# Kernel optimization log

Hardware: AMD Instinct MI355X
Metric: run time of the kernel (lower is better)

Reference implementation:

```python
import jax, jax.numpy as jnp
import numpy as np

N = 100000       # num nodes
E = 3200000      # num edges (avg degree 32)
F_IN = 128       # num_node_features
HID = 16         # hidden dim hard-coded in Net
C = 10           # num_classes


def setup_inputs() -> dict:
    key = jax.random.key(0)
    k1, k2, k3, k4 = jax.random.split(key, 4)
    x = jax.random.normal(k1, (N, F_IN), dtype=jnp.float32)
    edge_index = jax.random.randint(k2, (2, E), 0, N, dtype=jnp.int32)
    W1 = jax.random.normal(k3, (F_IN, HID), dtype=jnp.float32) * 0.05
    b1 = jnp.zeros((HID,), dtype=jnp.float32)
    W2 = jax.random.normal(k4, (HID, C), dtype=jnp.float32) * 0.05
    b2 = jnp.zeros((C,), dtype=jnp.float32)
    return {"x": x, "edge_index": edge_index, "W1": W1, "b1": b1, "W2": W2, "b2": b2}


def reference(x, edge_index, W1, b1, W2, b2):
    # GCNConv: out = D^{-1/2} (A + I) D^{-1/2} X W + b   (add self-loops)
    loops = jnp.arange(N, dtype=edge_index.dtype)
    row = jnp.concatenate([edge_index[0], loops])  # source nodes
    col = jnp.concatenate([edge_index[1], loops])  # target nodes

    # symmetric normalization (degrees include self-loops, so deg >= 1)
    deg = jax.ops.segment_sum(jnp.ones_like(col, dtype=jnp.float32), col, num_segments=N)
    dis = jax.lax.rsqrt(deg)
    norm = dis[row] * dis[col]  # [E+N]

    def gcn_conv(h, W, b):
        h = h @ W                               # [N, d_out] small GEMM first
        msg = h[row] * norm[:, None]            # gather + scale, [E+N, d_out]
        out = jax.ops.segment_sum(msg, col, num_segments=N)  # scatter-add
        return out + b

    h = jax.nn.relu(gcn_conv(x, W1, b1))
    # F.dropout(training=False) is identity in eval mode
    logits = gcn_conv(h, W2, b2)
    return jax.nn.log_softmax(logits, axis=1)
```

## Files before the change

kernel.cpp:

```cpp
#include <hip/hip_runtime.h>
#include <math.h>

#define N_NODES 100000
#define N_EDGES 3200000
#define F_IN 128
#define HID 16
#define C_OUT 10
#define WIN 256
#define NDIG 391
#define PNB2 500
#define EPB 6400
#define SCN (NDIG * PNB2)
#define SB1 764
#define MAXE2 20

typedef unsigned short u16;
typedef unsigned int u32;

__device__ __forceinline__ float bf2f(u16 u) {
    return __uint_as_float(((u32)u) << 16);
}
__device__ __forceinline__ u16 f2bf(float f) {
    u32 x = __float_as_uint(f);
    u32 r = (x + 0x7fffu + ((x >> 16) & 1u)) >> 16;
    return (u16)r;
}
__device__ __forceinline__ void acc8(float* a, uint4 w) {
    a[0] += bf2f((u16)(w.x & 0xffff)); a[1] += bf2f((u16)(w.x >> 16));
    a[2] += bf2f((u16)(w.y & 0xffff)); a[3] += bf2f((u16)(w.y >> 16));
    a[4] += bf2f((u16)(w.z & 0xffff)); a[5] += bf2f((u16)(w.z >> 16));
    a[6] += bf2f((u16)(w.w & 0xffff)); a[7] += bf2f((u16)(w.w >> 16));
}

__global__ void k_pcnt(const int* __restrict__ col, int* __restrict__ blkhistA) {
    __shared__ int h[NDIG];
    for (int i = threadIdx.x; i < NDIG; i += 256) h[i] = 0;
    __syncthreads();
    const uint4* c4 = (const uint4*)(col + blockIdx.x * EPB);
    for (int i = threadIdx.x; i < EPB / 4; i += 256) {
        uint4 c = c4[i];
        atomicAdd(&h[c.x >> 8], 1);
        atomicAdd(&h[c.y >> 8], 1);
        atomicAdd(&h[c.z >> 8], 1);
        atomicAdd(&h[c.w >> 8], 1);
    }
    __syncthreads();
    for (int d = threadIdx.x; d < NDIG; d += 256)
        blkhistA[d * PNB2 + blockIdx.x] = h[d];
}

__global__ void k_s1(const int* __restrict__ blkhistA, int* __restrict__ psum) {
    __shared__ int sm[256];
    int i = blockIdx.x * 256 + threadIdx.x;
    sm[threadIdx.x] = (i < SCN) ? blkhistA[i] : 0;
    __syncthreads();
    for (int off = 128; off > 0; off >>= 1) {
        if (threadIdx.x < off) sm[threadIdx.x] += sm[threadIdx.x + off];
        __syncthreads();
    }
    if (threadIdx.x == 0) psum[blockIdx.x] = sm[0];
}

__global__ void k_s3(const int* __restrict__ blkhistA, const int* __restrict__ psum,
                     int* __restrict__ blkhistB) {
    __shared__ int ps[1024];
    __shared__ int sm[256];
    int t = threadIdx.x;
    for (int i = t; i < 1024; i += 256) ps[i] = (i < SB1) ? psum[i] : 0;
    __syncthreads();
    for (int off = 1; off < 1024; off <<= 1) {
        int v[4];
#pragma unroll
        for (int j = 0; j < 4; j++) {
            int idx = t + j * 256;
            v[j] = ps[idx] + ((idx >= off) ? ps[idx - off] : 0);
        }
        __syncthreads();
#pragma unroll
        for (int j = 0; j < 4; j++) ps[t + j * 256] = v[j];
        __syncthreads();
    }
    int bpre = (blockIdx.x > 0) ? ps[blockIdx.x - 1] : 0;

    int i = blockIdx.x * 256 + t;
    int v = (i < SCN) ? blkhistA[i] : 0;
    sm[t] = v;
    __syncthreads();
    for (int off = 1; off < 256; off <<= 1) {
        int a = sm[t];
        int b = (t >= off) ? sm[t - off] : 0;
        __syncthreads();
        sm[t] = a + b;
        __syncthreads();
    }
    if (i < SCN) blkhistB[i] = bpre + sm[t] - v;
}

__global__ void __launch_bounds__(512) k_pwrite(
        const int* __restrict__ row, const int* __restrict__ col,
        const int* __restrict__ blkhistA, const int* __restrict__ blkhistB,
        u32* __restrict__ staging) {
    __shared__ u32 sorted[EPB];
    __shared__ u16 dwin[EPB];
    __shared__ int gbase[NDIG];
    __shared__ int lbase[NDIG];
    __shared__ int lcur[NDIG];
    __shared__ int scan[512];

    int t = threadIdx.x;
    int b = blockIdx.x;
    int hv = 0;
    if (t < NDIG) {
        hv = blkhistA[t * PNB2 + b];
        gbase[t] = blkhistB[t * PNB2 + b];
        lcur[t] = 0;
    }
    scan[t] = hv;
    __syncthreads();
    for (int off = 1; off < 512; off <<= 1) {
        int v = scan[t];
        int u = (t >= off) ? scan[t - off] : 0;
        __syncthreads();
        scan[t] = v + u;
        __syncthreads();
    }
    if (t < NDIG) lbase[t] = scan[t] - hv;
    __syncthreads();

    const uint4* c4 = (const uint4*)(col + b * EPB);
    const uint4* r4 = (const uint4*)(row + b * EPB);
    for (int i = t; i < EPB / 4; i += 512) {
        uint4 c = c4[i];
        uint4 r = r4[i];
        int d, rank, pos;
        d = (int)(c.x >> 8); rank = atomicAdd(&lcur[d], 1); pos = lbase[d] + rank;
        sorted[pos] = ((c.x & 255u) << 17) | r.x; dwin[pos] = (u16)d;
        d = (int)(c.y >> 8); rank = atomicAdd(&lcur[d], 1); pos = lbase[d] + rank;
        sorted[pos] = ((c.y & 255u) << 17) | r.y; dwin[pos] = (u16)d;
        d = (int)(c.z >> 8); rank = atomicAdd(&lcur[d], 1); pos = lbase[d] + rank;
        sorted[pos] = ((c.z & 255u) << 17) | r.z; dwin[pos] = (u16)d;
        d = (int)(c.w >> 8); rank = atomicAdd(&lcur[d], 1); pos = lbase[d] + rank;
        sorted[pos] = ((c.w & 255u) << 17) | r.w; dwin[pos] = (u16)d;
    }
    __syncthreads();

    for (int i = t; i < EPB; i += 512) {
        int d = dwin[i];
        staging[gbase[d] + (i - lbase[d])] = sorted[i];
    }
}

__global__ void __launch_bounds__(512) k_csr(
        u32* staging, const int* __restrict__ blkhistB,
        int* __restrict__ offs, float* __restrict__ dis) {
    __shared__ int cnt[WIN];
    __shared__ int base[WIN];
    int w = blockIdx.x;
    int t = threadIdx.x;
    if (t < WIN) cnt[t] = 0;
    __syncthreads();
    int start = blkhistB[w * PNB2];
    int end = (w == NDIG - 1) ? N_EDGES : blkhistB[(w + 1) * PNB2];
    u32 buf[MAXE2];
    int n = 0;
#pragma unroll
    for (int k = 0; k < MAXE2; k++) {
        int i = start + k * 512 + t;
        if (i < end) {
            u32 e = staging[i];
            buf[k] = e;
            n = k + 1;
            atomicAdd(&cnt[e >> 17], 1);
        }
    }
    __syncthreads();
    if (t < WIN) base[t] = cnt[t];
    __syncthreads();
    for (int off = 1; off < WIN; off <<= 1) {
        int v = 0;
        if (t < WIN) {
            v = base[t];
            if (t >= off) v += base[t - off];
        }
        __syncthreads();
        if (t < WIN) base[t] = v;
        __syncthreads();
    }
    if (t < WIN) {
        int excl = base[t] - cnt[t];
        base[t] = excl;
        int node = w * WIN + t;
        if (node < N_NODES) {
            offs[node] = start + excl;
            dis[node] = rsqrtf(1.0f + (float)cnt[t]);
        }
    }
    if (w == 0 && t == 0) offs[N_NODES] = N_EDGES;
    __syncthreads();
    if (t < WIN) cnt[t] = 0;
    __syncthreads();
#pragma unroll
    for (int k = 0; k < MAXE2; k++) {
        if (k < n) {
            u32 e = buf[k];
            int cl = (int)(e >> 17);
            int rank = atomicAdd(&cnt[cl], 1);
            staging[start + base[cl] + rank] = e;
        }
    }
}

__global__ void k_gemm1(const float* __restrict__ x, const float* __restrict__ W1,
                        const float* __restrict__ dis, u16* __restrict__ h1s) {
    __shared__ float Ws[F_IN * HID];
    for (int t = threadIdx.x; t < F_IN * HID; t += blockDim.x) Ws[t] = W1[t];
    __syncthreads();

    int node = blockIdx.x * blockDim.x + threadIdx.x;
    if (node >= N_NODES) return;

    float acc[HID];
#pragma unroll
    for (int j = 0; j < HID; j++) acc[j] = 0.f;

    const float4* xr = (const float4*)(x + (size_t)node * F_IN);
#pragma unroll 2
    for (int k4 = 0; k4 < F_IN / 4; k4++) {
        float4 v = xr[k4];
        float xv[4] = {v.x, v.y, v.z, v.w};
#pragma unroll
        for (int kk = 0; kk < 4; kk++) {
            const float4* wr = (const float4*)(Ws + (k4 * 4 + kk) * HID);
            float4 w0 = wr[0], w1 = wr[1], w2 = wr[2], w3 = wr[3];
            float xs = xv[kk];
            acc[0]  += xs * w0.x; acc[1]  += xs * w0.y; acc[2]  += xs * w0.z; acc[3]  += xs * w0.w;
            acc[4]  += xs * w1.x; acc[5]  += xs * w1.y; acc[6]  += xs * w1.z; acc[7]  += xs * w1.w;
            acc[8]  += xs * w2.x; acc[9]  += xs * w2.y; acc[10] += xs * w2.z; acc[11] += xs * w2.w;
            acc[12] += xs * w3.x; acc[13] += xs * w3.y; acc[14] += xs * w3.z; acc[15] += xs * w3.w;
        }
    }

    float d = dis[node];
    u32 p[8];
#pragma unroll
    for (int i = 0; i < 8; i++)
        p[i] = (u32)f2bf(acc[2 * i] * d) | ((u32)f2bf(acc[2 * i + 1] * d) << 16);
    u32* dst = (u32*)(h1s + (size_t)node * HID);
#pragma unroll
    for (int i = 0; i < 8; i++) dst[i] = p[i];
}

__global__ void k_gl1(const int* __restrict__ offs, const u32* __restrict__ csr,
                      const float* __restrict__ dis, const u16* __restrict__ h1s,
                      const float* __restrict__ b1, const float* __restrict__ W2,
                      u16* __restrict__ h2s) {
    __shared__ float Ws[HID * C_OUT];
    __shared__ float b1s[HID];
    if (threadIdx.x < HID * C_OUT) Ws[threadIdx.x] = W2[threadIdx.x];
    if (threadIdx.x < HID) b1s[threadIdx.x] = b1[threadIdx.x];
    __syncthreads();

    int t = blockIdx.x * 256 + threadIdx.x;
    if (t >= N_NODES * 4) return;
    int node = t >> 2;
    int q = t & 3;
    int half = q >> 1;
    int eh = q & 1;
    const uint4* hb = (const uint4*)h1s;
    float a[8] = {0.f, 0.f, 0.f, 0.f, 0.f, 0.f, 0.f, 0.f};
    if (eh == 0) acc8(a, hb[(size_t)node * 2 + half]);
    int o = offs[node + half];
    int oo = __shfl_xor(o, 2);
    int s0 = half ? oo : o;
    int s1 = half ? o : oo;
    int mid = s0 + ((s1 - s0) >> 1);
    int lo = eh ? mid : s0;
    int hi = eh ? s1 : mid;
    int j = lo;
    for (; j < hi && (j & 3); j++)
        acc8(a, hb[(size_t)(csr[j] & 0x1FFFFu) * 2 + half]);
    for (; j + 4 <= hi; j += 4) {
        uint4 ss = *(const uint4*)(csr + j);
        uint4 w0 = hb[(size_t)(ss.x & 0x1FFFFu) * 2 + half];
        uint4 w1 = hb[(size_t)(ss.y & 0x1FFFFu) * 2 + half];
        uint4 w2 = hb[(size_t)(ss.z & 0x1FFFFu) * 2 + half];
        uint4 w3 = hb[(size_t)(ss.w & 0x1FFFFu) * 2 + half];
        acc8(a, w0); acc8(a, w1); acc8(a, w2); acc8(a, w3);
    }
    for (; j < hi; j++)
        acc8(a, hb[(size_t)(csr[j] & 0x1FFFFu) * 2 + half]);

#pragma unroll
    for (int k = 0; k < 8; k++) a[k] += __shfl_xor(a[k], 1);

    float dc = dis[node];
    float own[8], oth[8];
#pragma unroll
    for (int k = 0; k < 8; k++) own[k] = a[k] * dc;
#pragma unroll
    for (int k = 0; k < 8; k++) oth[k] = __shfl_xor(own[k], 2);
    float h[16];
#pragma unroll
    for (int k = 0; k < 8; k++) {
        h[k]     = half ? oth[k] : own[k];
        h[8 + k] = half ? own[k] : oth[k];
    }
#pragma unroll
    for (int jj = 0; jj < 16; jj++) h[jj] = fmaxf(h[jj] + b1s[jj], 0.f);

    int nf = half ? 2 : 8;
    float outv[8];
#pragma unroll
    for (int k = 0; k < 8; k++) {
        float s = 0.f;
        if (k < nf) {
            int kk = half * 8 + k;
#pragma unroll
            for (int jj = 0; jj < 16; jj++) s += h[jj] * Ws[jj * C_OUT + kk];
        }
        outv[k] = s * dc;
    }
    if (eh == 0) {
        uint4 ov;
        ov.x = (u32)f2bf(outv[0]) | ((u32)f2bf(outv[1]) << 16);
        ov.y = half ? 0u : ((u32)f2bf(outv[2]) | ((u32)f2bf(outv[3]) << 16));
        ov.z = half ? 0u : ((u32)f2bf(outv[4]) | ((u32)f2bf(outv[5]) << 16));
        ov.w = half ? 0u : ((u32)f2bf(outv[6]) | ((u32)f2bf(outv[7]) << 16));
        ((uint4*)h2s)[(size_t)node * 2 + half] = ov;
    }
}

__global__ void k_gather2(const int* __restrict__ offs, const u32* __restrict__ csr,
                          const float* __restrict__ dis, const u16* __restrict__ h2s,
                          const float* __restrict__ b2, float* __restrict__ out) {
    __shared__ float b2s[C_OUT];
    if (threadIdx.x < C_OUT) b2s[threadIdx.x] = b2[threadIdx.x];
    __syncthreads();

    int t = blockIdx.x * 256 + threadIdx.x;
    if (t >= N_NODES * 4) return;
    int node = t >> 2;
    int q = t & 3;
    int half = q >> 1;
    int eh = q & 1;
    const uint4* hb = (const uint4*)h2s;
    float a[8] = {0.f, 0.f, 0.f, 0.f, 0.f, 0.f, 0.f, 0.f};
    if (eh == 0) acc8(a, hb[(size_t)node * 2 + half]);
    int o = offs[node + half];
    int oo = __shfl_xor(o, 2);
    int s0 = half ? oo : o;
    int s1 = half ? o : oo;
    int mid = s0 + ((s1 - s0) >> 1);
    int lo = eh ? mid : s0;
    int hi = eh ? s1 : mid;
    int j = lo;
    for (; j < hi && (j & 3); j++)
        acc8(a, hb[(size_t)(csr[j] & 0x1FFFFu) * 2 + half]);
    for (; j + 4 <= hi; j += 4) {
        uint4 ss = *(const uint4*)(csr + j);
        uint4 w0 = hb[(size_t)(ss.x & 0x1FFFFu) * 2 + half];
        uint4 w1 = hb[(size_t)(ss.y & 0x1FFFFu) * 2 + half];
        uint4 w2 = hb[(size_t)(ss.z & 0x1FFFFu) * 2 + half];
        uint4 w3 = hb[(size_t)(ss.w & 0x1FFFFu) * 2 + half];
        acc8(a, w0); acc8(a, w1); acc8(a, w2); acc8(a, w3);
    }
    for (; j < hi; j++)
        acc8(a, hb[(size_t)(csr[j] & 0x1FFFFu) * 2 + half]);

#pragma unroll
    for (int k = 0; k < 8; k++) a[k] += __shfl_xor(a[k], 1);

    float dc = dis[node];
    int nf = half ? 2 : 8;
    float lg[8];
    float m = -1e30f;
#pragma unroll
    for (int k = 0; k < 8; k++) {
        lg[k] = a[k] * dc + b2s[(half * 8 + k) % C_OUT];
        if (k < nf) m = fmaxf(m, lg[k]);
    }
    m = fmaxf(m, __shfl_xor(m, 2));
    float s = 0.f;
#pragma unroll
    for (int k = 0; k < 8; k++)
        if (k < nf) s += expf(lg[k] - m);
    s += __shfl_xor(s, 2);
    float ls = logf(s) + m;
    if (eh == 0) {
        float* dst = out + (size_t)node * C_OUT + half * 8;
        if (half == 0) {
#pragma unroll
            for (int i = 0; i < 4; i++)
                *(float2*)(dst + 2 * i) = make_float2(lg[2 * i] - ls, lg[2 * i + 1] - ls);
        } else {
            *(float2*)dst = make_float2(lg[0] - ls, lg[1] - ls);
        }
    }
}

extern "C" void kernel_launch(void* const* d_in, const int* in_sizes, int n_in,
                              void* d_out, int out_size, void* d_ws, size_t ws_size,
                              hipStream_t stream) {
    const float* x  = (const float*)d_in[0];
    const int*   ei = (const int*)d_in[1];
    const float* W1 = (const float*)d_in[2];
    const float* b1 = (const float*)d_in[3];
    const float* W2 = (const float*)d_in[4];
    const float* b2 = (const float*)d_in[5];
    float* out = (float*)d_out;

    const int* row = ei;
    const int* col = ei + N_EDGES;

    char* ws = (char*)d_ws;
    float* dis      = (float*)(ws);
    int*   offs     = (int*)(ws + 400000);
    int*   blkhistA = (int*)(ws + 800016);
    int*   blkhistB = (int*)(ws + 1582352);
    int*   psum     = (int*)(ws + 2364688);
    u32*   staging  = (u32*)(ws + 2367744);
    u16*   h1s      = (u16*)(ws + 15167744);
    u16*   h2s      = (u16*)(ws + 18367744);

    const int B = 256;
    int gN  = (N_NODES + B - 1) / B;
    int gN4 = (N_NODES * 4 + B - 1) / B;

    k_pcnt  <<<PNB2, B, 0, stream>>>(col, blkhistA);
    k_s1    <<<SB1, B, 0, stream>>>(blkhistA, psum);
    k_s3    <<<SB1, B, 0, stream>>>(blkhistA, psum, blkhistB);
    k_pwrite<<<PNB2, 512, 0, stream>>>(row, col, blkhistA, blkhistB, staging);
    k_csr   <<<NDIG, 512, 0, stream>>>(staging, blkhistB, offs, dis);
    k_gemm1 <<<gN, B, 0, stream>>>(x, W1, dis, h1s);
    k_gl1   <<<gN4, B, 0, stream>>>(offs, staging, dis, h1s, b1, W2, h2s);
    k_gather2<<<gN4, B, 0, stream>>>(offs, staging, dis, h2s, b2, out);
}
```

Before: 222.8 us.

## Split edge gather over four lanes per half-row and stage CSR sort in LDS

Result: faster. 212.2 us (-4.8%).

```diff
diff --git a/kernel.cpp b/kernel.cpp
--- a/kernel.cpp
+++ b/kernel.cpp
@@ -13,6 +13,7 @@
 #define SCN (NDIG * PNB2)
 #define SB1 764
 #define MAXE2 20
+#define CSRLDS 10240
 
 typedef unsigned short u16;
 typedef unsigned int u32;
@@ -153,6 +154,7 @@
 __global__ void __launch_bounds__(512) k_csr(
         u32* staging, const int* __restrict__ blkhistB,
         int* __restrict__ offs, float* __restrict__ dis) {
+    __shared__ u32 sorted[CSRLDS];
     __shared__ int cnt[WIN];
     __shared__ int base[WIN];
     int w = blockIdx.x;
@@ -161,13 +163,14 @@
     __syncthreads();
     int start = blkhistB[w * PNB2];
     int end = (w == NDIG - 1) ? N_EDGES : blkhistB[(w + 1) * PNB2];
+    int m = end - start;
     u32 buf[MAXE2];
     int n = 0;
 #pragma unroll
     for (int k = 0; k < MAXE2; k++) {
-        int i = start + k * 512 + t;
-        if (i < end) {
-            u32 e = staging[i];
+        int i = k * 512 + t;
+        if (i < m) {
+            u32 e = staging[start + i];
             buf[k] = e;
             n = k + 1;
             atomicAdd(&cnt[e >> 17], 1);
@@ -197,17 +200,17 @@
     }
     if (w == 0 && t == 0) offs[N_NODES] = N_EDGES;
     __syncthreads();
-    if (t < WIN) cnt[t] = 0;
-    __syncthreads();
 #pragma unroll
     for (int k = 0; k < MAXE2; k++) {
         if (k < n) {
             u32 e = buf[k];
-            int cl = (int)(e >> 17);
-            int rank = atomicAdd(&cnt[cl], 1);
-            staging[start + base[cl] + rank] = e;
-        }
-    }
+            int pos = atomicAdd(&base[(int)(e >> 17)], 1);
+            sorted[pos] = e;
+        }
+    }
+    __syncthreads();
+    for (int i = t; i < m; i += 512)
+        staging[start + i] = sorted[i];
 }
 
 __global__ void k_gemm1(const float* __restrict__ x, const float* __restrict__ W1,
@@ -261,21 +264,21 @@
     __syncthreads();
 
     int t = blockIdx.x * 256 + threadIdx.x;
-    if (t >= N_NODES * 4) return;
-    int node = t >> 2;
-    int q = t & 3;
-    int half = q >> 1;
-    int eh = q & 1;
+    if (t >= N_NODES * 8) return;
+    int node = t >> 3;
+    int q = t & 7;
+    int half = q >> 2;
+    int eq = q & 3;
     const uint4* hb = (const uint4*)h1s;
     float a[8] = {0.f, 0.f, 0.f, 0.f, 0.f, 0.f, 0.f, 0.f};
-    if (eh == 0) acc8(a, hb[(size_t)node * 2 + half]);
+    if (eq == 0) acc8(a, hb[(size_t)node * 2 + half]);
     int o = offs[node + half];
-    int oo = __shfl_xor(o, 2);
+    int oo = __shfl_xor(o, 4);
     int s0 = half ? oo : o;
     int s1 = half ? o : oo;
-    int mid = s0 + ((s1 - s0) >> 1);
-    int lo = eh ? mid : s0;
-    int hi = eh ? s1 : mid;
+    int len = s1 - s0;
+    int lo = s0 + ((len * eq) >> 2);
+    int hi = s0 + ((len * (eq + 1)) >> 2);
     int j = lo;
     for (; j < hi && (j & 3); j++)
         acc8(a, hb[(size_t)(csr[j] & 0x1FFFFu) * 2 + half]);
@@ -291,14 +294,17 @@
         acc8(a, hb[(size_t)(csr[j] & 0x1FFFFu) * 2 + half]);
 
 #pragma unroll
-    for (int k = 0; k < 8; k++) a[k] += __shfl_xor(a[k], 1);
+    for (int k = 0; k < 8; k++) {
+        a[k] += __shfl_xor(a[k], 1);
+        a[k] += __shfl_xor(a[k], 2);
+    }
 
     float dc = dis[node];
     float own[8], oth[8];
 #pragma unroll
     for (int k = 0; k < 8; k++) own[k] = a[k] * dc;
 #pragma unroll
-    for (int k = 0; k < 8; k++) oth[k] = __shfl_xor(own[k], 2);
+    for (int k = 0; k < 8; k++) oth[k] = __shfl_xor(own[k], 4);
     float h[16];
 #pragma unroll
     for (int k = 0; k < 8; k++) {
@@ -320,7 +326,7 @@
         }
         outv[k] = s * dc;
     }
-    if (eh == 0) {
+    if (eq == 0) {
         uint4 ov;
         ov.x = (u32)f2bf(outv[0]) | ((u32)f2bf(outv[1]) << 16);
         ov.y = half ? 0u : ((u32)f2bf(outv[2]) | ((u32)f2bf(outv[3]) << 16));
@@ -338,21 +344,21 @@
     __syncthreads();
 
     int t = blockIdx.x * 256 + threadIdx.x;
-    if (t >= N_NODES * 4) return;
-    int node = t >> 2;
-    int q = t & 3;
-    int half = q >> 1;
-    int eh = q & 1;
+    if (t >= N_NODES * 8) return;
+    int node = t >> 3;
+    int q = t & 7;
+    int half = q >> 2;
+    int eq = q & 3;
     const uint4* hb = (const uint4*)h2s;
     float a[8] = {0.f, 0.f, 0.f, 0.f, 0.f, 0.f, 0.f, 0.f};
-    if (eh == 0) acc8(a, hb[(size_t)node * 2 + half]);
+    if (eq == 0) acc8(a, hb[(size_t)node * 2 + half]);
     int o = offs[node + half];
-    int oo = __shfl_xor(o, 2);
+    int oo = __shfl_xor(o, 4);
     int s0 = half ? oo : o;
     int s1 = half ? o : oo;
-    int mid = s0 + ((s1 - s0) >> 1);
-    int lo = eh ? mid : s0;
-    int hi = eh ? s1 : mid;
+    int len = s1 - s0;
+    int lo = s0 + ((len * eq) >> 2);
+    int hi = s0 + ((len * (eq + 1)) >> 2);
     int j = lo;
     for (; j < hi && (j & 3); j++)
         acc8(a, hb[(size_t)(csr[j] & 0x1FFFFu) * 2 + half]);
@@ -368,7 +374,10 @@
         acc8(a, hb[(size_t)(csr[j] & 0x1FFFFu) * 2 + half]);
 
 #pragma unroll
-    for (int k = 0; k < 8; k++) a[k] += __shfl_xor(a[k], 1);
+    for (int k = 0; k < 8; k++) {
+        a[k] += __shfl_xor(a[k], 1);
+        a[k] += __shfl_xor(a[k], 2);
+    }
 
     float dc = dis[node];
     int nf = half ? 2 : 8;
@@ -379,14 +388,14 @@
         lg[k] = a[k] * dc + b2s[(half * 8 + k) % C_OUT];
         if (k < nf) m = fmaxf(m, lg[k]);
     }
-    m = fmaxf(m, __shfl_xor(m, 2));
+    m = fmaxf(m, __shfl_xor(m, 4));
     float s = 0.f;
 #pragma unroll
     for (int k = 0; k < 8; k++)
         if (k < nf) s += expf(lg[k] - m);
-    s += __shfl_xor(s, 2);
+    s += __shfl_xor(s, 4);
     float ls = logf(s) + m;
-    if (eh == 0) {
+    if (eq == 0) {
         float* dst = out + (size_t)node * C_OUT + half * 8;
         if (half == 0) {
 #pragma unroll
@@ -424,7 +433,7 @@
 
     const int B = 256;
     int gN  = (N_NODES + B - 1) / B;
-    int gN4 = (N_NODES * 4 + B - 1) / B;
+    int gN8 = (N_NODES * 8 + B - 1) / B;
 
     k_pcnt  <<<PNB2, B, 0, stream>>>(col, blkhistA);
     k_s1    <<<SB1, B, 0, stream>>>(blkhistA, psum);
@@ -432,6 +441,6 @@
     k_pwrite<<<PNB2, 512, 0, stream>>>(row, col, blkhistA, blkhistB, staging);
     k_csr   <<<NDIG, 512, 0, stream>>>(staging, blkhistB, offs, dis);
     k_gemm1 <<<gN, B, 0, stream>>>(x, W1, dis, h1s);
-    k_gl1   <<<gN4, B, 0, stream>>>(offs, staging, dis, h1s, b1, W2, h2s);
-    k_gather2<<<gN4, B, 0, stream>>>(offs, staging, dis, h2s, b2, out);
-}
+    k_gl1   <<<gN8, B, 0, stream>>>(offs, staging, dis, h1s, b1, W2, h2s);
+    k_gather2<<<gN8, B, 0, stream>>>(offs, staging, dis, h2s, b2, out);
+}
```
